# Performance work log

Measured on AMD Instinct MI355X. Metric: run time of the kernel, lower is better.

The kernel has to match this reference:

```python
import jax, jax.numpy as jnp
import numpy as np

D_MODEL = 1024
SCALE = float(np.sqrt(D_MODEL))


def setup_inputs() -> dict:
    key = jax.random.key(0)
    k1, k2, k3 = jax.random.split(key, 3)
    input_data = jax.random.normal(k1, (4, 2048, D_MODEL), dtype=jnp.float32)
    qk = jax.random.normal(k2, (D_MODEL, D_MODEL), dtype=jnp.float32) / SCALE
    ov = jax.random.normal(k3, (D_MODEL, D_MODEL), dtype=jnp.float32) / SCALE
    return {"input_data": input_data, "qk": qk, "ov": ov}


def reference(input_data, qk, ov):
    # input_data: [B, S, D]; qk, ov: [D, D]
    S = input_data.shape[1]
    # scores: [B, S, S] = (x @ qk) @ x^T / sqrt(D)
    scores = jnp.einsum("bsd,de,bte->bst", input_data, qk, input_data) / SCALE
    # causal mask: positions t > s get -inf (upper triangle, diagonal=1)
    causal = jnp.tril(jnp.ones((S, S), dtype=bool))
    scores = jnp.where(causal, scores, -jnp.inf)
    attn = jax.nn.softmax(scores, axis=-1)
    # A: [B, S, D] = attn @ x @ ov
    return jnp.einsum("bst,btd,de->bse", attn, input_data, ov)
```

## Files before the change

### kernel.cpp

```cpp
#include <hip/hip_runtime.h>
#include <hip/hip_bf16.h>
#include <cstdint>
#include <cstddef>


using bf16 = __hip_bfloat16;
typedef __attribute__((ext_vector_type(8))) short short8;
typedef __attribute__((ext_vector_type(4))) float f32x4;

#define NB 4
#define SS 2048
#define DD 1024

__device__ __forceinline__ void async_lds16(const bf16* g, bf16* l) {
  __builtin_amdgcn_global_load_lds(
      (const __attribute__((address_space(1))) void*)g,
      (__attribute__((address_space(3))) void*)l,
      16, 0, 0);
}

struct alignas(8) bf16x4s { bf16 a, b, c, d; };

__global__ __launch_bounds__(256) void prep_kernel(const float* __restrict__ x,
                                                   bf16* __restrict__ xb,
                                                   const float* __restrict__ qk,
                                                   bf16* __restrict__ qkT,
                                                   const float* __restrict__ ov,
                                                   bf16* __restrict__ ovT,
                                                   float* __restrict__ l) {
  __shared__ bf16 tile[64][65];
  const int bx = blockIdx.x;
  if (bx < 8192) {
    int i = (bx * 256 + threadIdx.x) * 4;
    float4 v = *(const float4*)(x + i);
    bf16x4s o{__float2bfloat16(v.x), __float2bfloat16(v.y),
              __float2bfloat16(v.z), __float2bfloat16(v.w)};
    *(bf16x4s*)(xb + i) = o;
  } else if (bx < 8704) {
    const int idx = bx - 8192;
    const float* in = (idx & 256) ? ov : qk;
    bf16* out = (idx & 256) ? ovT : qkT;
    const int rem = idx & 255;
    const int tbx = (rem & 15) * 64;
    const int tby = (rem >> 4) * 64;
    const int tc = threadIdx.x & 63;
    const int tr = threadIdx.x >> 6;
#pragma unroll
    for (int r = tr; r < 64; r += 4)
      tile[tc][r] = __float2bfloat16(in[(size_t)(tby + r) * DD + tbx + tc]);
    __syncthreads();
#pragma unroll
    for (int r = tr; r < 64; r += 4)
      out[(size_t)(tbx + r) * DD + tby + tc] = tile[r][tc];
  } else {
    const int t = (bx - 8704) * 256 + threadIdx.x;
    f32x4 z = {0.f, 0.f, 0.f, 0.f};
    *(f32x4*)(l + t * 4) = z;
  }
}

template <int EPI, int STAGES>
__device__ __forceinline__ void gemm_core(const bf16* __restrict__ Ab,
                                          const bf16* __restrict__ Bb,
                                          void* __restrict__ C,
                                          int N, int K, int m0, int n0, int nk,
                                          bf16* As, bf16* Bs,
                                          float* __restrict__ l) {
  const int tid  = threadIdx.x;
  const int lane = tid & 63;
  const int wave = tid >> 6;
  const int wm   = (wave >> 1) << 6;
  const int wn   = (wave & 1) << 6;
  const int quad = lane >> 4;
  const int r    = lane & 15;

  f32x4 zero = {0.f, 0.f, 0.f, 0.f};
  f32x4 acc[4][4];
#pragma unroll
  for (int i = 0; i < 4; ++i)
#pragma unroll
    for (int j = 0; j < 4; ++j) acc[i][j] = zero;

  const long long aoff = (long long)(m0 + (tid >> 2)) * K + (tid & 3) * 8;
  const long long boff = (long long)(n0 + (tid >> 2)) * K + (tid & 3) * 8;

  auto stage = [&](int kt, int s) {
    const long long k0 = (long long)kt << 5;
    bf16* lA = As + s * 4096 + wave * 512;
    bf16* lB = Bs + s * 4096 + wave * 512;
    async_lds16(Ab + aoff + k0, lA);
    async_lds16(Ab + aoff + 64LL * K + k0, lA + 2048);
    async_lds16(Bb + boff + k0, lB);
    async_lds16(Bb + boff + 64LL * K + k0, lB + 2048);
  };

  stage(0, 0);
  if (STAGES == 3 && nk > 1) stage(1, 1);

  int s = 0;
  for (int kt = 0; kt < nk; ++kt) {
    if (STAGES == 3) {
      if (kt + 2 < nk) {
        int s2 = s + 2; if (s2 >= 3) s2 -= 3;
        stage(kt + 2, s2);
        asm volatile("s_waitcnt vmcnt(8)" ::: "memory");
      } else if (kt + 1 < nk) {
        asm volatile("s_waitcnt vmcnt(4)" ::: "memory");
      } else {
        asm volatile("s_waitcnt vmcnt(0)" ::: "memory");
      }
    } else {
      if (kt + 1 < nk) {
        stage(kt + 1, s ^ 1);
        asm volatile("s_waitcnt vmcnt(4)" ::: "memory");
      } else {
        asm volatile("s_waitcnt vmcnt(0)" ::: "memory");
      }
    }
    asm volatile("s_barrier" ::: "memory");

    const bf16* Ak = As + s * 4096;
    const bf16* Bk = Bs + s * 4096;
    short8 af[4], bfr[4];
#pragma unroll
    for (int i = 0; i < 4; ++i)
      af[i] = *(const short8*)(Ak + (wm + i * 16 + r) * 32 + quad * 8);
#pragma unroll
    for (int i = 0; i < 4; ++i)
      bfr[i] = *(const short8*)(Bk + (wn + i * 16 + r) * 32 + quad * 8);
#pragma unroll
    for (int i = 0; i < 4; ++i)
#pragma unroll
      for (int j = 0; j < 4; ++j)
        acc[i][j] = __builtin_amdgcn_mfma_f32_16x16x32_bf16(af[i], bfr[j], acc[i][j], 0, 0, 0);

    asm volatile("s_barrier" ::: "memory");
    if (STAGES == 3) { if (++s == 3) s = 0; } else { s ^= 1; }
  }

#pragma unroll
  for (int i = 0; i < 4; ++i) {
    const int row0 = m0 + wm + i * 16 + quad * 4;
    if (EPI == 1) {
#pragma unroll
      for (int j = 0; j < 4; ++j) {
        const int col = n0 + wn + j * 16 + r;
#pragma unroll
        for (int q = 0; q < 4; ++q)
          ((bf16*)C)[(long long)(row0 + q) * N + col] = __float2bfloat16(acc[i][j][q]);
      }
    } else if (EPI == 2) {
      float qs[4] = {0.f, 0.f, 0.f, 0.f};
#pragma unroll
      for (int j = 0; j < 4; ++j) {
        const int col = n0 + wn + j * 16 + r;
#pragma unroll
        for (int q = 0; q < 4; ++q) {
          const int row = row0 + q;
          float v = (col <= row) ? __expf(acc[i][j][q] * 0.03125f) : 0.0f;
          ((bf16*)C)[(long long)row * N + col] = __float2bfloat16(v);
          qs[q] += v;
        }
      }
#pragma unroll
      for (int q = 0; q < 4; ++q) {
#pragma unroll
        for (int off = 1; off < 16; off <<= 1) qs[q] += __shfl_xor(qs[q], off, 64);
        if (r == 0) atomicAdd(&l[row0 + q], qs[q]);
      }
    } else {
      float rs[4];
#pragma unroll
      for (int q = 0; q < 4; ++q) rs[q] = 1.0f / l[row0 + q];
#pragma unroll
      for (int j = 0; j < 4; ++j) {
        const int col = n0 + wn + j * 16 + r;
#pragma unroll
        for (int q = 0; q < 4; ++q)
          ((float*)C)[(long long)(row0 + q) * N + col] = acc[i][j][q] * rs[q];
      }
    }
  }
}

__global__ __launch_bounds__(256) void gemm_qv(const bf16* __restrict__ xb,
                                               const bf16* __restrict__ qkT,
                                               const bf16* __restrict__ ovT,
                                               bf16* __restrict__ Qb,
                                               bf16* __restrict__ Vt) {
  __shared__ bf16 As[3 * 4096];
  __shared__ bf16 Bs[3 * 4096];
  const long long SD = (long long)SS * DD;
  const int z = blockIdx.z;
  if (z < 4) {
    const int by = blockIdx.x & 15, bx = blockIdx.x >> 4;
    gemm_core<1, 3>(xb + z * SD, qkT, Qb + z * SD, DD, DD, by * 128, bx * 128, 32, As, Bs, nullptr);
  } else {
    const int bx = blockIdx.x & 15, by = blockIdx.x >> 4;
    gemm_core<1, 3>(ovT, xb + (z - 4) * SD, Vt + (z - 4) * SD, SS, DD, by * 128, bx * 128, 32, As, Bs, nullptr);
  }
}

__global__ __launch_bounds__(256) void gemm_sc(const bf16* __restrict__ Qb,
                                               const bf16* __restrict__ xb,
                                               bf16* __restrict__ P,
                                               float* __restrict__ l) {
  __shared__ bf16 As[2 * 4096];
  __shared__ bf16 Bs[2 * 4096];
  const long long SD = (long long)SS * DD;
  const long long SSQ = (long long)SS * SS;
  const int t = blockIdx.x;
  int bm = (int)((sqrtf(8.0f * (float)t + 1.0f) - 1.0f) * 0.5f);
  while ((bm + 1) * (bm + 2) / 2 <= t) ++bm;
  while (bm * (bm + 1) / 2 > t) --bm;
  const int bn = t - bm * (bm + 1) / 2;
  const int b = blockIdx.z;
  gemm_core<2, 2>(Qb + b * SD, xb + b * SD, P + b * SSQ, SS, DD, bm * 128, bn * 128, 32,
                  As, Bs, l + b * SS);
}

__global__ __launch_bounds__(256) void gemm_pv(const bf16* __restrict__ P,
                                               const bf16* __restrict__ Vt,
                                               const float* __restrict__ l,
                                               float* __restrict__ out) {
  __shared__ bf16 As[2 * 4096];
  __shared__ bf16 Bs[2 * 4096];
  const long long SD = (long long)SS * DD;
  const long long SSQ = (long long)SS * SS;
  const int bm = 15 - blockIdx.y;
  const int m0 = bm * 128;
  const int nk = (m0 + 128) >> 5;
  const int b = blockIdx.z;
  gemm_core<3, 2>(P + b * SSQ, Vt + b * SD, out + b * SD, DD, SS, m0, blockIdx.x * 128, nk,
                  As, Bs, (float*)l + b * SS);
}

extern "C" void kernel_launch(void* const* d_in, const int* in_sizes, int n_in,
                              void* d_out, int out_size, void* d_ws, size_t ws_size,
                              hipStream_t stream) {
  const float* x  = (const float*)d_in[0];
  const float* qk = (const float*)d_in[1];
  const float* ov = (const float*)d_in[2];
  float* out = (float*)d_out;

  char* ws = (char*)d_ws;
  const size_t MB = 1ull << 20;
  bf16*  xb  = (bf16*)(ws + 0);
  bf16*  qkT = (bf16*)(ws + 16 * MB);
  bf16*  ovT = (bf16*)(ws + 18 * MB);
  bf16*  Qb  = (bf16*)(ws + 20 * MB);
  bf16*  Vt  = (bf16*)(ws + 36 * MB);
  bf16*  P   = (bf16*)(ws + 52 * MB);
  float* l   = (float*)(ws + 84 * MB);

  prep_kernel<<<dim3(8712), 256, 0, stream>>>(x, xb, qk, qkT, ov, ovT, l);
  gemm_qv<<<dim3(128, 1, 8), 256, 0, stream>>>(xb, qkT, ovT, Qb, Vt);
  gemm_sc<<<dim3(136, 1, 4), 256, 0, stream>>>(Qb, xb, P, l);
  gemm_pv<<<dim3(8, 16, 4), 256, 0, stream>>>(P, Vt, l, out);
}
```

Baseline: 229.5 us.

## Halve M-tile to 64 rows for score and PV GEMMs, use 3-stage pipeline

Adds an IT template parameter so gemm_core can run with 64-row A tiles. The causal score GEMM and the PV GEMM now launch twice as many blocks, each covering 64x128, with triangle index mapping and K bounds adjusted to match. Both also move from a 2-stage to a 3-stage LDS pipeline. The goal is more blocks and better occupancy and load balance across CUs on the triangular workload, and less wasted work on the diagonal in PV. In exchange, each block reuses its B tile less, so more B traffic goes to L2.

```diff
diff --git a/kernel.cpp b/kernel.cpp
--- a/kernel.cpp
+++ b/kernel.cpp
@@ -59,7 +59,7 @@
   }
 }
 
-template <int EPI, int STAGES>
+template <int EPI, int STAGES, int IT>
 __device__ __forceinline__ void gemm_core(const bf16* __restrict__ Ab,
                                           const bf16* __restrict__ Bb,
                                           void* __restrict__ C,
@@ -69,15 +69,16 @@
   const int tid  = threadIdx.x;
   const int lane = tid & 63;
   const int wave = tid >> 6;
-  const int wm   = (wave >> 1) << 6;
+  const int wm   = (wave >> 1) * (IT * 16);
   const int wn   = (wave & 1) << 6;
   const int quad = lane >> 4;
   const int r    = lane & 15;
+  const int ASZ  = IT * 1024;
 
   f32x4 zero = {0.f, 0.f, 0.f, 0.f};
-  f32x4 acc[4][4];
-#pragma unroll
-  for (int i = 0; i < 4; ++i)
+  f32x4 acc[IT][4];
+#pragma unroll
+  for (int i = 0; i < IT; ++i)
 #pragma unroll
     for (int j = 0; j < 4; ++j) acc[i][j] = zero;
 
@@ -86,10 +87,10 @@
 
   auto stage = [&](int kt, int s) {
     const long long k0 = (long long)kt << 5;
-    bf16* lA = As + s * 4096 + wave * 512;
+    bf16* lA = As + s * ASZ + wave * 512;
     bf16* lB = Bs + s * 4096 + wave * 512;
     async_lds16(Ab + aoff + k0, lA);
-    async_lds16(Ab + aoff + 64LL * K + k0, lA + 2048);
+    if (IT == 4) async_lds16(Ab + aoff + 64LL * K + k0, lA + 2048);
     async_lds16(Bb + boff + k0, lB);
     async_lds16(Bb + boff + 64LL * K + k0, lB + 2048);
   };
@@ -99,47 +100,50 @@
 
   int s = 0;
   for (int kt = 0; kt < nk; ++kt) {
-    if (STAGES == 3) {
+    if constexpr (STAGES == 3) {
       if (kt + 2 < nk) {
         int s2 = s + 2; if (s2 >= 3) s2 -= 3;
         stage(kt + 2, s2);
-        asm volatile("s_waitcnt vmcnt(8)" ::: "memory");
+        if constexpr (IT == 4) asm volatile("s_waitcnt vmcnt(8)" ::: "memory");
+        else                   asm volatile("s_waitcnt vmcnt(6)" ::: "memory");
       } else if (kt + 1 < nk) {
-        asm volatile("s_waitcnt vmcnt(4)" ::: "memory");
+        if constexpr (IT == 4) asm volatile("s_waitcnt vmcnt(4)" ::: "memory");
+        else                   asm volatile("s_waitcnt vmcnt(3)" ::: "memory");
       } else {
         asm volatile("s_waitcnt vmcnt(0)" ::: "memory");
       }
     } else {
       if (kt + 1 < nk) {
         stage(kt + 1, s ^ 1);
-        asm volatile("s_waitcnt vmcnt(4)" ::: "memory");
+        if constexpr (IT == 4) asm volatile("s_waitcnt vmcnt(4)" ::: "memory");
+        else                   asm volatile("s_waitcnt vmcnt(3)" ::: "memory");
       } else {
         asm volatile("s_waitcnt vmcnt(0)" ::: "memory");
       }
     }
     asm volatile("s_barrier" ::: "memory");
 
-    const bf16* Ak = As + s * 4096;
+    const bf16* Ak = As + s * ASZ;
     const bf16* Bk = Bs + s * 4096;
-    short8 af[4], bfr[4];
-#pragma unroll
-    for (int i = 0; i < 4; ++i)
+    short8 af[IT], bfr[4];
+#pragma unroll
+    for (int i = 0; i < IT; ++i)
       af[i] = *(const short8*)(Ak + (wm + i * 16 + r) * 32 + quad * 8);
 #pragma unroll
-    for (int i = 0; i < 4; ++i)
-      bfr[i] = *(const short8*)(Bk + (wn + i * 16 + r) * 32 + quad * 8);
-#pragma unroll
-    for (int i = 0; i < 4; ++i)
+    for (int j = 0; j < 4; ++j)
+      bfr[j] = *(const short8*)(Bk + (wn + j * 16 + r) * 32 + quad * 8);
+#pragma unroll
+    for (int i = 0; i < IT; ++i)
 #pragma unroll
       for (int j = 0; j < 4; ++j)
         acc[i][j] = __builtin_amdgcn_mfma_f32_16x16x32_bf16(af[i], bfr[j], acc[i][j], 0, 0, 0);
 
     asm volatile("s_barrier" ::: "memory");
-    if (STAGES == 3) { if (++s == 3) s = 0; } else { s ^= 1; }
-  }
-
-#pragma unroll
-  for (int i = 0; i < 4; ++i) {
+    if constexpr (STAGES == 3) { if (++s == 3) s = 0; } else { s ^= 1; }
+  }
+
+#pragma unroll
+  for (int i = 0; i < IT; ++i) {
     const int row0 = m0 + wm + i * 16 + quad * 4;
     if (EPI == 1) {
 #pragma unroll
@@ -194,10 +198,10 @@
   const int z = blockIdx.z;
   if (z < 4) {
     const int by = blockIdx.x & 15, bx = blockIdx.x >> 4;
-    gemm_core<1, 3>(xb + z * SD, qkT, Qb + z * SD, DD, DD, by * 128, bx * 128, 32, As, Bs, nullptr);
+    gemm_core<1, 3, 4>(xb + z * SD, qkT, Qb + z * SD, DD, DD, by * 128, bx * 128, 32, As, Bs, nullptr);
   } else {
     const int bx = blockIdx.x & 15, by = blockIdx.x >> 4;
-    gemm_core<1, 3>(ovT, xb + (z - 4) * SD, Vt + (z - 4) * SD, SS, DD, by * 128, bx * 128, 32, As, Bs, nullptr);
+    gemm_core<1, 3, 4>(ovT, xb + (z - 4) * SD, Vt + (z - 4) * SD, SS, DD, by * 128, bx * 128, 32, As, Bs, nullptr);
   }
 }
 
@@ -205,34 +209,36 @@
                                                const bf16* __restrict__ xb,
                                                bf16* __restrict__ P,
                                                float* __restrict__ l) {
-  __shared__ bf16 As[2 * 4096];
-  __shared__ bf16 Bs[2 * 4096];
+  __shared__ bf16 As[3 * 2048];
+  __shared__ bf16 Bs[3 * 4096];
   const long long SD = (long long)SS * DD;
   const long long SSQ = (long long)SS * SS;
   const int t = blockIdx.x;
-  int bm = (int)((sqrtf(8.0f * (float)t + 1.0f) - 1.0f) * 0.5f);
-  while ((bm + 1) * (bm + 2) / 2 <= t) ++bm;
-  while (bm * (bm + 1) / 2 > t) --bm;
-  const int bn = t - bm * (bm + 1) / 2;
+  int p = (int)sqrtf((float)t);
+  while (p * (p + 1) > t) --p;
+  while ((p + 1) * (p + 2) <= t) ++p;
+  int bm, bn;
+  if (t < (p + 1) * (p + 1)) { bm = 2 * p;     bn = t - p * (p + 1); }
+  else                       { bm = 2 * p + 1; bn = t - (p + 1) * (p + 1); }
   const int b = blockIdx.z;
-  gemm_core<2, 2>(Qb + b * SD, xb + b * SD, P + b * SSQ, SS, DD, bm * 128, bn * 128, 32,
-                  As, Bs, l + b * SS);
+  gemm_core<2, 3, 2>(Qb + b * SD, xb + b * SD, P + b * SSQ, SS, DD, bm * 64, bn * 128, 32,
+                     As, Bs, l + b * SS);
 }
 
 __global__ __launch_bounds__(256) void gemm_pv(const bf16* __restrict__ P,
                                                const bf16* __restrict__ Vt,
                                                const float* __restrict__ l,
                                                float* __restrict__ out) {
-  __shared__ bf16 As[2 * 4096];
-  __shared__ bf16 Bs[2 * 4096];
+  __shared__ bf16 As[3 * 2048];
+  __shared__ bf16 Bs[3 * 4096];
   const long long SD = (long long)SS * DD;
   const long long SSQ = (long long)SS * SS;
-  const int bm = 15 - blockIdx.y;
-  const int m0 = bm * 128;
-  const int nk = (m0 + 128) >> 5;
+  const int bm = 31 - blockIdx.y;
+  const int m0 = bm * 64;
+  const int nk = ((m0 >> 7) + 1) * 4;
   const int b = blockIdx.z;
-  gemm_core<3, 2>(P + b * SSQ, Vt + b * SD, out + b * SD, DD, SS, m0, blockIdx.x * 128, nk,
-                  As, Bs, (float*)l + b * SS);
+  gemm_core<3, 3, 2>(P + b * SSQ, Vt + b * SD, out + b * SD, DD, SS, m0, blockIdx.x * 128, nk,
+                     As, Bs, (float*)l + b * SS);
 }
 
 extern "C" void kernel_launch(void* const* d_in, const int* in_sizes, int n_in,
@@ -255,6 +261,6 @@
 
   prep_kernel<<<dim3(8712), 256, 0, stream>>>(x, xb, qk, qkT, ov, ovT, l);
   gemm_qv<<<dim3(128, 1, 8), 256, 0, stream>>>(xb, qkT, ovT, Qb, Vt);
-  gemm_sc<<<dim3(136, 1, 4), 256, 0, stream>>>(Qb, xb, P, l);
-  gemm_pv<<<dim3(8, 16, 4), 256, 0, stream>>>(P, Vt, l, out);
-}
+  gemm_sc<<<dim3(272, 1, 4), 256, 0, stream>>>(Qb, xb, P, l);
+  gemm_pv<<<dim3(8, 32, 4), 256, 0, stream>>>(P, Vt, l, out);
+}
```

New measurement: 238.1 us. 3.7% more time.

## Fuse all stages into one cooperative persistent kernel with grid syncs

Applied to the files above, without the earlier changes.

Replaces the four separate launches (prep, QV gemm, score gemm, PV gemm) with a single cooperative kernel of 1024 blocks that runs each stage in turn and separates them with grid.sync(). The aim is to remove kernel launch gaps and inter-kernel drain/fill costs. The fused kernel drops the GEMMs from 3-stage to 2-stage LDS pipelining so that four blocks fit per CU, which may weaken latency hiding. Grid-wide barriers also idle blocks during the unbalanced later stages, since only 544 and 512 of the 1024 blocks have work there. A fallback to the old multi-kernel path is kept for when the occupancy query or cooperative launch fails.

```diff
diff --git a/kernel.cpp b/kernel.cpp
--- a/kernel.cpp
+++ b/kernel.cpp
@@ -1,9 +1,12 @@
 #include <hip/hip_runtime.h>
+#include <hip/hip_cooperative_groups.h>
 #include <hip/hip_bf16.h>
 #include <cstdint>
 #include <cstddef>
 
 
+namespace cg = cooperative_groups;
+
 using bf16 = __hip_bfloat16;
 typedef __attribute__((ext_vector_type(8))) short short8;
 typedef __attribute__((ext_vector_type(4))) float f32x4;
@@ -11,6 +14,7 @@
 #define NB 4
 #define SS 2048
 #define DD 1024
+#define MEGA_GRID 1024
 
 __device__ __forceinline__ void async_lds16(const bf16* g, bf16* l) {
   __builtin_amdgcn_global_load_lds(
@@ -20,44 +24,6 @@
 }
 
 struct alignas(8) bf16x4s { bf16 a, b, c, d; };
-
-__global__ __launch_bounds__(256) void prep_kernel(const float* __restrict__ x,
-                                                   bf16* __restrict__ xb,
-                                                   const float* __restrict__ qk,
-                                                   bf16* __restrict__ qkT,
-                                                   const float* __restrict__ ov,
-                                                   bf16* __restrict__ ovT,
-                                                   float* __restrict__ l) {
-  __shared__ bf16 tile[64][65];
-  const int bx = blockIdx.x;
-  if (bx < 8192) {
-    int i = (bx * 256 + threadIdx.x) * 4;
-    float4 v = *(const float4*)(x + i);
-    bf16x4s o{__float2bfloat16(v.x), __float2bfloat16(v.y),
-              __float2bfloat16(v.z), __float2bfloat16(v.w)};
-    *(bf16x4s*)(xb + i) = o;
-  } else if (bx < 8704) {
-    const int idx = bx - 8192;
-    const float* in = (idx & 256) ? ov : qk;
-    bf16* out = (idx & 256) ? ovT : qkT;
-    const int rem = idx & 255;
-    const int tbx = (rem & 15) * 64;
-    const int tby = (rem >> 4) * 64;
-    const int tc = threadIdx.x & 63;
-    const int tr = threadIdx.x >> 6;
-#pragma unroll
-    for (int r = tr; r < 64; r += 4)
-      tile[tc][r] = __float2bfloat16(in[(size_t)(tby + r) * DD + tbx + tc]);
-    __syncthreads();
-#pragma unroll
-    for (int r = tr; r < 64; r += 4)
-      out[(size_t)(tbx + r) * DD + tby + tc] = tile[r][tc];
-  } else {
-    const int t = (bx - 8704) * 256 + threadIdx.x;
-    f32x4 z = {0.f, 0.f, 0.f, 0.f};
-    *(f32x4*)(l + t * 4) = z;
-  }
-}
 
 template <int EPI, int STAGES>
 __device__ __forceinline__ void gemm_core(const bf16* __restrict__ Ab,
@@ -99,7 +65,7 @@
 
   int s = 0;
   for (int kt = 0; kt < nk; ++kt) {
-    if (STAGES == 3) {
+    if constexpr (STAGES == 3) {
       if (kt + 2 < nk) {
         int s2 = s + 2; if (s2 >= 3) s2 -= 3;
         stage(kt + 2, s2);
@@ -126,8 +92,8 @@
     for (int i = 0; i < 4; ++i)
       af[i] = *(const short8*)(Ak + (wm + i * 16 + r) * 32 + quad * 8);
 #pragma unroll
-    for (int i = 0; i < 4; ++i)
-      bfr[i] = *(const short8*)(Bk + (wn + i * 16 + r) * 32 + quad * 8);
+    for (int j = 0; j < 4; ++j)
+      bfr[j] = *(const short8*)(Bk + (wn + j * 16 + r) * 32 + quad * 8);
 #pragma unroll
     for (int i = 0; i < 4; ++i)
 #pragma unroll
@@ -135,7 +101,7 @@
         acc[i][j] = __builtin_amdgcn_mfma_f32_16x16x32_bf16(af[i], bfr[j], acc[i][j], 0, 0, 0);
 
     asm volatile("s_barrier" ::: "memory");
-    if (STAGES == 3) { if (++s == 3) s = 0; } else { s ^= 1; }
+    if constexpr (STAGES == 3) { if (++s == 3) s = 0; } else { s ^= 1; }
   }
 
 #pragma unroll
@@ -181,6 +147,112 @@
       }
     }
   }
+}
+
+__device__ __forceinline__ void prep_job(int job, const float* x, bf16* xb,
+                                         const float* qk, bf16* qkT,
+                                         const float* ov, bf16* ovT,
+                                         float* l, bf16* smem) {
+  if (job < 8192) {
+    int i = (job * 256 + (int)threadIdx.x) * 4;
+    float4 v = *(const float4*)(x + i);
+    bf16x4s o{__float2bfloat16(v.x), __float2bfloat16(v.y),
+              __float2bfloat16(v.z), __float2bfloat16(v.w)};
+    *(bf16x4s*)(xb + i) = o;
+  } else if (job < 8704) {
+    bf16 (*tile)[65] = (bf16(*)[65])smem;
+    const int idx = job - 8192;
+    const float* in = (idx & 256) ? ov : qk;
+    bf16* outp = (idx & 256) ? ovT : qkT;
+    const int rem = idx & 255;
+    const int tbx = (rem & 15) * 64;
+    const int tby = (rem >> 4) * 64;
+    const int tc = threadIdx.x & 63;
+    const int tr = threadIdx.x >> 6;
+#pragma unroll
+    for (int r = tr; r < 64; r += 4)
+      tile[tc][r] = __float2bfloat16(in[(size_t)(tby + r) * DD + tbx + tc]);
+    __syncthreads();
+#pragma unroll
+    for (int r = tr; r < 64; r += 4)
+      outp[(size_t)(tbx + r) * DD + tby + tc] = tile[r][tc];
+    __syncthreads();
+  } else {
+    const int t = (job - 8704) * 256 + (int)threadIdx.x;
+    f32x4 z = {0.f, 0.f, 0.f, 0.f};
+    *(f32x4*)(l + t * 4) = z;
+  }
+}
+
+__global__ __launch_bounds__(256, 4) void mega_kernel(
+    const float* __restrict__ x,  bf16* __restrict__ xb,
+    const float* __restrict__ qk, bf16* __restrict__ qkT,
+    const float* __restrict__ ov, bf16* __restrict__ ovT,
+    float* __restrict__ l,
+    bf16* __restrict__ Qb, bf16* __restrict__ Vt,
+    bf16* __restrict__ P,  float* __restrict__ out) {
+  cg::grid_group grid = cg::this_grid();
+
+  __shared__ bf16 smem[4 * 4096];
+  bf16* As = smem;
+  bf16* Bs = smem + 2 * 4096;
+
+  const long long SD = (long long)SS * DD;
+  const long long SSQ = (long long)SS * SS;
+
+  for (int job = blockIdx.x; job < 8712; job += MEGA_GRID)
+    prep_job(job, x, xb, qk, qkT, ov, ovT, l, smem);
+  grid.sync();
+
+  {
+    const int job = blockIdx.x;
+    const int z = job >> 7;
+    const int xj = job & 127;
+    if (z < 4) {
+      const int by = xj & 15, bx = xj >> 4;
+      gemm_core<1, 2>(xb + z * SD, qkT, Qb + z * SD, DD, DD, by * 128, bx * 128, 32, As, Bs, nullptr);
+    } else {
+      const int bx = xj & 15, by = xj >> 4;
+      gemm_core<1, 2>(ovT, xb + (z - 4) * SD, Vt + (z - 4) * SD, SS, DD, by * 128, bx * 128, 32, As, Bs, nullptr);
+    }
+  }
+  grid.sync();
+
+  if (blockIdx.x < 544) {
+    const int job = blockIdx.x;
+    const int b = job / 136;
+    const int t = job - b * 136;
+    int bm = (int)((sqrtf(8.0f * (float)t + 1.0f) - 1.0f) * 0.5f);
+    while ((bm + 1) * (bm + 2) / 2 <= t) ++bm;
+    while (bm * (bm + 1) / 2 > t) --bm;
+    const int bn = t - bm * (bm + 1) / 2;
+    gemm_core<2, 2>(Qb + b * SD, xb + b * SD, P + b * SSQ, SS, DD, bm * 128, bn * 128, 32,
+                    As, Bs, l + b * SS);
+  }
+  grid.sync();
+
+  if (blockIdx.x < 512) {
+    const int job = blockIdx.x;
+    const int bx = job & 7;
+    const int by = (job >> 3) & 15;
+    const int b = job >> 7;
+    const int bm = 15 - by;
+    const int m0 = bm * 128;
+    const int nk = (m0 + 128) >> 5;
+    gemm_core<3, 2>(P + b * SSQ, Vt + b * SD, out + b * SD, DD, SS, m0, bx * 128, nk,
+                    As, Bs, (float*)l + b * SS);
+  }
+}
+
+__global__ __launch_bounds__(256) void prep_kernel(const float* __restrict__ x,
+                                                   bf16* __restrict__ xb,
+                                                   const float* __restrict__ qk,
+                                                   bf16* __restrict__ qkT,
+                                                   const float* __restrict__ ov,
+                                                   bf16* __restrict__ ovT,
+                                                   float* __restrict__ l) {
+  __shared__ bf16 smem[64 * 66];
+  prep_job(blockIdx.x, x, xb, qk, qkT, ov, ovT, l, smem);
 }
 
 __global__ __launch_bounds__(256) void gemm_qv(const bf16* __restrict__ xb,
@@ -253,6 +325,21 @@
   bf16*  P   = (bf16*)(ws + 52 * MB);
   float* l   = (float*)(ws + 84 * MB);
 
+  int occ = 0;
+  hipError_t qerr = hipOccupancyMaxActiveBlocksPerMultiprocessor(
+      &occ, (const void*)mega_kernel, 256, 0);
+  bool coop_ok = (qerr == hipSuccess && occ >= 4);
+
+  if (coop_ok) {
+    void* args[] = {(void*)&x, (void*)&xb, (void*)&qk, (void*)&qkT,
+                    (void*)&ov, (void*)&ovT, (void*)&l,
+                    (void*)&Qb, (void*)&Vt, (void*)&P, (void*)&out};
+    hipError_t lerr = hipLaunchCooperativeKernel((const void*)mega_kernel,
+                                                 dim3(MEGA_GRID), dim3(256),
+                                                 args, 0, stream);
+    if (lerr == hipSuccess) return;
+  }
+
   prep_kernel<<<dim3(8712), 256, 0, stream>>>(x, xb, qk, qkT, ov, ovT, l);
   gemm_qv<<<dim3(128, 1, 8), 256, 0, stream>>>(xb, qkT, ovT, Qb, Vt);
   gemm_sc<<<dim3(136, 1, 4), 256, 0, stream>>>(Qb, xb, P, l);
```

New measurement: 230.3 us. About the same (+0.3%).
